# Kernel optimization log

Measured on AMD Instinct MI355X. Metric: run time of the kernel, lower is better.

Reference implementation:

```python
import jax, jax.numpy as jnp
import numpy as np

B, S, D, H = 2, 4096, 256, 4
DH = D // H  # head dim = 64


def setup_inputs() -> dict:
    key = jax.random.key(0)
    ks = jax.random.split(key, 7)
    scale = 1.0 / np.sqrt(D)
    return {
        "x": jax.random.normal(ks[0], (B, S, D), dtype=jnp.float32),
        "Wq": jax.random.normal(ks[1], (D, D), dtype=jnp.float32) * scale,
        "bq": jax.random.normal(ks[2], (D,), dtype=jnp.float32) * scale,
        "Wk": jax.random.normal(ks[3], (D, D), dtype=jnp.float32) * scale,
        "bk": jax.random.normal(ks[4], (D,), dtype=jnp.float32) * scale,
        "Wv": jax.random.normal(ks[5], (D, D), dtype=jnp.float32) * scale,
        "bv": jax.random.normal(ks[6], (D,), dtype=jnp.float32) * scale,
    }


def reference(x, Wq, bq, Wk, bk, Wv, bv):
    b, s, d = x.shape
    # torch Linear: y = x @ W.T + b ; W stored as [out, in]
    q = (jnp.einsum('bsd,ed->bse', x, Wq) + bq).reshape(b, s, H, DH)
    k = (jnp.einsum('bsd,ed->bse', x, Wk) + bk).reshape(b, s, H, DH)
    v = (jnp.einsum('bsd,ed->bse', x, Wv) + bv).reshape(b, s, H, DH)
    # scores: [b, s(query), t(key), h]
    scores = jnp.einsum('bshd,bthd->bsth', q, k) / jnp.sqrt(jnp.float32(DH))
    # softmax over key axis t (dim=-2 in torch layout bsth)
    weights = jax.nn.softmax(scores, axis=2)
    out = jnp.einsum('bsth,bthd->bshd', weights, v)
    return out.reshape(b, s, d)
```

## Files before the change

### kernel.cpp

```cpp
#include <hip/hip_runtime.h>

#define S_LEN 4096
#define D_MODEL 256
#define NH 4
#define DH 64
#define CSC 0.18033688011112042f
#define FRAG 520

typedef __attribute__((ext_vector_type(8))) short bf16x8;
typedef __attribute__((ext_vector_type(8))) unsigned short u16x8;
typedef __attribute__((ext_vector_type(4))) float f32x4;
typedef __attribute__((ext_vector_type(16))) float f32x16;
typedef __attribute__((ext_vector_type(2))) unsigned int u32x2;
typedef __attribute__((ext_vector_type(4))) unsigned int u32x4;

#define MFMA16(a, b, c) __builtin_amdgcn_mfma_f32_16x16x32_bf16((a), (b), (c), 0, 0, 0)
#define MFMA32(a, b, c) __builtin_amdgcn_mfma_f32_32x32x16_bf16((a), (b), (c), 0, 0, 0)

static __device__ __forceinline__ unsigned short f2bf(float f) {
  unsigned int u = __float_as_uint(f);
  u += 0x7fffu + ((u >> 16) & 1u);
  return (unsigned short)(u >> 16);
}

static __device__ __forceinline__ unsigned int cvtpk(float lo, float hi) {
  unsigned int r;
  asm("v_cvt_pk_bf16_f32 %0, %1, %2" : "=v"(r) : "v"(lo), "v"(hi));
  return r;
}

static __device__ __forceinline__ u16x8 cvt8(float4 a, float4 b) {
  u16x8 v;
  v[0] = f2bf(a.x); v[1] = f2bf(a.y); v[2] = f2bf(a.z); v[3] = f2bf(a.w);
  v[4] = f2bf(b.x); v[5] = f2bf(b.y); v[6] = f2bf(b.z); v[7] = f2bf(b.w);
  return v;
}

static __device__ __forceinline__ void pack_pb(const f32x16& s0, const f32x16& s1,
                                               bf16x8* pb) {
  unsigned int u0[8], u1[8];
#pragma unroll
  for (int gg = 0; gg < 4; ++gg) {
    u0[gg * 2 + 0] = cvtpk(s0[4 * gg + 0], s0[4 * gg + 1]);
    u0[gg * 2 + 1] = cvtpk(s0[4 * gg + 2], s0[4 * gg + 3]);
    u1[gg * 2 + 0] = cvtpk(s1[4 * gg + 0], s1[4 * gg + 1]);
    u1[gg * 2 + 1] = cvtpk(s1[4 * gg + 2], s1[4 * gg + 3]);
  }
#pragma unroll
  for (int S = 0; S < 2; ++S) {
    u32x2 w0 = __builtin_amdgcn_permlane32_swap(u0[4 * S + 0], u0[4 * S + 2], false, false);
    u32x2 w1 = __builtin_amdgcn_permlane32_swap(u0[4 * S + 1], u0[4 * S + 3], false, false);
    u32x4 t0; t0[0] = w0[0]; t0[1] = w1[0]; t0[2] = w0[1]; t0[3] = w1[1];
    pb[S] = __builtin_bit_cast(bf16x8, t0);
    u32x2 w2 = __builtin_amdgcn_permlane32_swap(u1[4 * S + 0], u1[4 * S + 2], false, false);
    u32x2 w3 = __builtin_amdgcn_permlane32_swap(u1[4 * S + 1], u1[4 * S + 3], false, false);
    u32x4 t1; t1[0] = w2[0]; t1[1] = w3[0]; t1[2] = w2[1]; t1[3] = w3[1];
    pb[2 + S] = __builtin_bit_cast(bf16x8, t1);
  }
}

__global__ __launch_bounds__(256) void prep(
    const float* __restrict__ Wq, const float* __restrict__ Wk,
    const float* __restrict__ Wv, unsigned short* __restrict__ Wb)
{
  const int gid = blockIdx.x * 256 + threadIdx.x;
  const int l   = gid & 63;
  const int f   = gid >> 6;
  const int kk  = f & 7;
  const int ctn = f >> 3;
  const int ct  = ctn & 3, nt = ctn >> 2;
  const int pj  = nt >> 2, h = nt & 3;
  const float* Wsel = (pj == 0) ? Wq : (pj == 1) ? Wk : Wv;
  const float* src =
      Wsel + (size_t)(h * 64 + ct * 16 + (l & 15)) * D_MODEL + kk * 32 + (l >> 4) * 8;
  float4 a = *(const float4*)src;
  float4 b = *(const float4*)(src + 4);
  *(u16x8*)(Wb + (size_t)gid * 8) = cvt8(a, b);
}

__global__ __launch_bounds__(256) void qkv_proj(
    const float* __restrict__ x, const unsigned short* __restrict__ Wb,
    const float* __restrict__ bq, const float* __restrict__ bk,
    const float* __restrict__ bv,
    unsigned short* __restrict__ Qh, unsigned short* __restrict__ Kh,
    unsigned short* __restrict__ Vt)
{
  __shared__ unsigned short xs[32][264];
  __shared__ float tbuf[32][68];

  const int tid  = threadIdx.x;
  const int lane = tid & 63;
  const int w    = tid >> 6;
  const int r16  = lane & 15;
  const int hi   = lane >> 4;
  const int m0   = (blockIdx.x >> 1) * 32;
  const int ntB  = (blockIdx.x & 1) * 6;

  {
    const int r  = tid >> 3;
    const int c0 = (tid & 7) * 32;
    const float* xp = x + (size_t)(m0 + r) * D_MODEL + c0;
#pragma unroll
    for (int i = 0; i < 32; i += 8) {
      float4 a = *(const float4*)(xp + i);
      float4 b = *(const float4*)(xp + i + 4);
      *(u16x8*)&xs[r][c0 + i] = cvt8(a, b);
    }
  }
  __syncthreads();

  const int bb = m0 >> 12;
  const int s_base = m0 & 4095;

  for (int t = 0; t < 6; ++t) {
    const int nt = ntB + t, pj = nt >> 2, h = nt & 3;
    f32x4 acc[2] = {};
    const size_t fb = (size_t)(nt * 4 + w) * 8;
#pragma unroll
    for (int kk = 0; kk < 8; ++kk) {
      bf16x8 bw = *(const bf16x8*)(Wb + (fb + kk) * 512 + lane * 8);
#pragma unroll
      for (int rt = 0; rt < 2; ++rt) {
        bf16x8 af = *(const bf16x8*)&xs[rt * 16 + r16][kk * 32 + hi * 8];
        acc[rt] = MFMA16(af, bw, acc[rt]);
      }
    }
    const float* bsel = (pj == 0) ? bq : (pj == 1) ? bk : bv;
    const float bias = bsel[h * 64 + w * 16 + r16];
    const float scl  = (pj == 0) ? CSC : 1.0f;

#pragma unroll
    for (int rt = 0; rt < 2; ++rt)
#pragma unroll
      for (int j = 0; j < 4; ++j)
        tbuf[rt * 16 + hi * 4 + j][w * 16 + r16] = (acc[rt][j] + bias) * scl;
    __syncthreads();

    if (pj < 2) {
      const int s_l = tid >> 3, c0 = (tid & 7) * 8;
      float4 a = *(const float4*)&tbuf[s_l][c0];
      float4 b = *(const float4*)&tbuf[s_l][c0 + 4];
      unsigned short* dst = ((pj == 0) ? Qh : Kh) +
          ((size_t)(bb * NH + h) * S_LEN + s_base + s_l) * DH + c0;
      *(u16x8*)dst = cvt8(a, b);
    } else {
      const int d_l = tid & 63, sblk = (tid >> 6) * 8;
      u16x8 vv;
#pragma unroll
      for (int e = 0; e < 8; ++e) vv[e] = f2bf(tbuf[sblk + e][d_l]);
      unsigned short* dst = Vt +
          ((size_t)(bb * NH + h) * DH + d_l) * S_LEN + s_base + sblk;
      *(u16x8*)dst = vv;
    }
    __syncthreads();
  }
}

__global__ __launch_bounds__(1024) void attn(
    const unsigned short* __restrict__ Qh,
    const unsigned short* __restrict__ Kh,
    const unsigned short* __restrict__ Vt,
    float* __restrict__ out)
{
  __shared__ unsigned short KV[2][2][4][8 * FRAG];

  const int tid = threadIdx.x;
  const int ln  = tid & 63;
  const int wv  = tid >> 6;
  const int g   = wv >> 2;
  const int wq  = wv & 3;
  const int r32 = ln & 31;
  const int h   = ln >> 5;

  const int bid = blockIdx.x;
  const int bh  = bid & 7;
  const int q0  = (bid >> 3) * 128;

  const unsigned short* Qb = Qh + (size_t)bh * S_LEN * DH;
  const unsigned short* Kb = Kh + (size_t)bh * S_LEN * DH;
  const unsigned short* Vb = Vt + (size_t)bh * DH * S_LEN;

  const int q = q0 + wq * 32 + r32;
  bf16x8 qf[4];
#pragma unroll
  for (int s = 0; s < 4; ++s)
    qf[s] = *(const bf16x8*)(Qb + (size_t)q * DH + s * 16 + h * 8);

  f32x16 o0 = {}, o1 = {};
  float l_run = 0.f;

  const int u  = tid & 255;
  const int gs = tid >> 8;
  const int sr = u >> 2;
  const int sc = (u & 3) * 16;
  const int f0   = (sc >> 4) * 2 + (sr >> 5);
  const int offA = f0 * FRAG + (sr & 31) * 8;
  const int offB = offA + 256;

  uint4 kA, kB, vA, vB;
#define LOAD_CHUNK(c)                                                          \
  { const unsigned short* kp = Kb + ((size_t)(c) * 64 + sr) * DH + sc;         \
    kA = *(const uint4*)kp;  kB = *(const uint4*)(kp + 8);                     \
    const unsigned short* vp = Vb + (size_t)sr * S_LEN + (c) * 64 + sc;        \
    vA = *(const uint4*)vp;  vB = *(const uint4*)(vp + 8); }
#define STAGE(par)                                                             \
  { unsigned short* kd = &KV[par][0][gs][0];                                   \
    *(uint4*)(kd + offA) = kA;  *(uint4*)(kd + offB) = kB;                     \
    unsigned short* vd = &KV[par][1][gs][0];                                   \
    *(uint4*)(vd + offA) = vA;  *(uint4*)(vd + offB) = vB; }

  LOAD_CHUNK(gs);
  STAGE(0);
  LOAD_CHUNK(4 + gs);

  for (int it = 0; it < 16; ++it) {
    __syncthreads();
    const unsigned short* Kc = &KV[it & 1][0][g][0];
    const unsigned short* Vc = &KV[it & 1][1][g][0];
    const int lb = ln * 8;

    f32x16 s0 = {}, s1 = {};
    __builtin_amdgcn_s_setprio(1);
#pragma unroll
    for (int s = 0; s < 4; ++s) {
      bf16x8 a0 = *(const bf16x8*)(Kc + lb + (2 * s + 0) * FRAG);
      bf16x8 a1 = *(const bf16x8*)(Kc + lb + (2 * s + 1) * FRAG);
      s0 = MFMA32(a0, qf[s], s0);
      s1 = MFMA32(a1, qf[s], s1);
    }
    __builtin_amdgcn_s_setprio(0);

    float pa = 0.f, pbs = 0.f, pc = 0.f, pd = 0.f;
#pragma unroll
    for (int i = 0; i < 16; i += 2) {
      s0[i]     = __builtin_amdgcn_exp2f(s0[i]);      pa  += s0[i];
      s0[i + 1] = __builtin_amdgcn_exp2f(s0[i + 1]);  pbs += s0[i + 1];
      s1[i]     = __builtin_amdgcn_exp2f(s1[i]);      pc  += s1[i];
      s1[i + 1] = __builtin_amdgcn_exp2f(s1[i + 1]);  pd  += s1[i + 1];
    }
    l_run += (pa + pbs) + (pc + pd);

    if (it < 15) {
      STAGE((it + 1) & 1);
      int c = 4 * (it + 2) + gs;  if (c > 63) c = 63;
      LOAD_CHUNK(c);
    }

    bf16x8 pb[4];
    pack_pb(s0, s1, pb);

    __builtin_amdgcn_s_setprio(1);
#pragma unroll
    for (int s = 0; s < 4; ++s) {
      bf16x8 b0 = *(const bf16x8*)(Vc + lb + (2 * s + 0) * FRAG);
      bf16x8 b1 = *(const bf16x8*)(Vc + lb + (2 * s + 1) * FRAG);
      o0 = MFMA32(b0, pb[s], o0);
      o1 = MFMA32(b1, pb[s], o1);
    }
    __builtin_amdgcn_s_setprio(0);
  }

  __syncthreads();
  float* cb = (float*)&KV[0][0][0][0];
  const int cbase = wq * 64 + ln;

  if (g >= 2) {
    const int base = ((g - 2) * 256 + cbase) * 33;
#pragma unroll
    for (int i = 0; i < 16; ++i) { cb[base + i] = o0[i]; cb[base + 16 + i] = o1[i]; }
    cb[base + 32] = l_run;
  }
  __syncthreads();
  if (g < 2) {
    const int base = (g * 256 + cbase) * 33;
#pragma unroll
    for (int i = 0; i < 16; ++i) { o0[i] += cb[base + i]; o1[i] += cb[base + 16 + i]; }
    l_run += cb[base + 32];
  }
  __syncthreads();
  if (g == 1) {
    const int base = cbase * 33;
#pragma unroll
    for (int i = 0; i < 16; ++i) { cb[base + i] = o0[i]; cb[base + 16 + i] = o1[i]; }
    cb[base + 32] = l_run;
  }
  __syncthreads();
  if (g == 0) {
    const int base = cbase * 33;
#pragma unroll
    for (int i = 0; i < 16; ++i) { o0[i] += cb[base + i]; o1[i] += cb[base + 16 + i]; }
    l_run += cb[base + 32];

    const float lt  = l_run + __shfl_xor(l_run, 32);
    const float inv = 1.f / lt;
    const int bb = bh >> 2, hd = bh & 3;
    float* op = out + ((size_t)(bb * S_LEN + q)) * D_MODEL + hd * DH;
#pragma unroll
    for (int gg = 0; gg < 4; ++gg) {
      float4 v0, v1;
      v0.x = o0[4 * gg + 0] * inv;  v0.y = o0[4 * gg + 1] * inv;
      v0.z = o0[4 * gg + 2] * inv;  v0.w = o0[4 * gg + 3] * inv;
      *(float4*)(op + 8 * gg + 4 * h) = v0;
      v1.x = o1[4 * gg + 0] * inv;  v1.y = o1[4 * gg + 1] * inv;
      v1.z = o1[4 * gg + 2] * inv;  v1.w = o1[4 * gg + 3] * inv;
      *(float4*)(op + 32 + 8 * gg + 4 * h) = v1;
    }
  }
}

extern "C" void kernel_launch(void* const* d_in, const int* in_sizes, int n_in,
                              void* d_out, int out_size, void* d_ws, size_t ws_size,
                              hipStream_t stream) {
  const float* x  = (const float*)d_in[0];
  const float* Wq = (const float*)d_in[1];
  const float* bq = (const float*)d_in[2];
  const float* Wk = (const float*)d_in[3];
  const float* bk = (const float*)d_in[4];
  const float* Wv = (const float*)d_in[5];
  const float* bv = (const float*)d_in[6];
  float* out = (float*)d_out;

  const size_t per = (size_t)2 * NH * S_LEN * DH;
  if (ws_size < 3 * per * sizeof(unsigned short)) return;
  unsigned short* Qh = (unsigned short*)d_ws;
  unsigned short* Kh = Qh + per;
  unsigned short* Vt = Kh + per;
  unsigned short* Wb = (unsigned short*)d_out;

  prep<<<96, 256, 0, stream>>>(Wq, Wk, Wv, Wb);
  qkv_proj<<<512, 256, 0, stream>>>(x, Wb, bq, bk, bv, Qh, Kh, Vt);
  attn<<<256, 1024, 0, stream>>>(Qh, Kh, Vt, out);
}
```

Before: 62.10 us.

## Split attention tile into halves to overlap exp/pack with MFMA; double qkv grid

The attention inner loop now computes the two 32-key score halves separately. It exponentiates and packs the first half and runs its PV MFMAs before doing the softmax of the second half, so transcendental work on one half can interleave with matrix ops on the other. The global-load staging is moved between the two halves. Separately, the QKV projection grid doubles to 1024 blocks, each handling 3 tiles instead of 6, which adds parallelism at the cost of reloading the x tile twice as often.

```diff
diff --git a/kernel.cpp b/kernel.cpp
--- a/kernel.cpp
+++ b/kernel.cpp
@@ -36,26 +36,19 @@
   return v;
 }
 
-static __device__ __forceinline__ void pack_pb(const f32x16& s0, const f32x16& s1,
-                                               bf16x8* pb) {
-  unsigned int u0[8], u1[8];
+static __device__ __forceinline__ void pack_half(const f32x16& s, bf16x8* pb) {
+  unsigned int u[8];
 #pragma unroll
   for (int gg = 0; gg < 4; ++gg) {
-    u0[gg * 2 + 0] = cvtpk(s0[4 * gg + 0], s0[4 * gg + 1]);
-    u0[gg * 2 + 1] = cvtpk(s0[4 * gg + 2], s0[4 * gg + 3]);
-    u1[gg * 2 + 0] = cvtpk(s1[4 * gg + 0], s1[4 * gg + 1]);
-    u1[gg * 2 + 1] = cvtpk(s1[4 * gg + 2], s1[4 * gg + 3]);
+    u[gg * 2 + 0] = cvtpk(s[4 * gg + 0], s[4 * gg + 1]);
+    u[gg * 2 + 1] = cvtpk(s[4 * gg + 2], s[4 * gg + 3]);
   }
 #pragma unroll
   for (int S = 0; S < 2; ++S) {
-    u32x2 w0 = __builtin_amdgcn_permlane32_swap(u0[4 * S + 0], u0[4 * S + 2], false, false);
-    u32x2 w1 = __builtin_amdgcn_permlane32_swap(u0[4 * S + 1], u0[4 * S + 3], false, false);
+    u32x2 w0 = __builtin_amdgcn_permlane32_swap(u[4 * S + 0], u[4 * S + 2], false, false);
+    u32x2 w1 = __builtin_amdgcn_permlane32_swap(u[4 * S + 1], u[4 * S + 3], false, false);
     u32x4 t0; t0[0] = w0[0]; t0[1] = w1[0]; t0[2] = w0[1]; t0[3] = w1[1];
     pb[S] = __builtin_bit_cast(bf16x8, t0);
-    u32x2 w2 = __builtin_amdgcn_permlane32_swap(u1[4 * S + 0], u1[4 * S + 2], false, false);
-    u32x2 w3 = __builtin_amdgcn_permlane32_swap(u1[4 * S + 1], u1[4 * S + 3], false, false);
-    u32x4 t1; t1[0] = w2[0]; t1[1] = w3[0]; t1[2] = w2[1]; t1[3] = w3[1];
-    pb[2 + S] = __builtin_bit_cast(bf16x8, t1);
   }
 }
 
@@ -93,8 +86,8 @@
   const int w    = tid >> 6;
   const int r16  = lane & 15;
   const int hi   = lane >> 4;
-  const int m0   = (blockIdx.x >> 1) * 32;
-  const int ntB  = (blockIdx.x & 1) * 6;
+  const int m0   = (blockIdx.x >> 2) * 32;
+  const int ntB  = (blockIdx.x & 3) * 3;
 
   {
     const int r  = tid >> 3;
@@ -112,7 +105,7 @@
   const int bb = m0 >> 12;
   const int s_base = m0 & 4095;
 
-  for (int t = 0; t < 6; ++t) {
+  for (int t = 0; t < 3; ++t) {
     const int nt = ntB + t, pj = nt >> 2, h = nt & 3;
     f32x4 acc[2] = {};
     const size_t fb = (size_t)(nt * 4 + w) * 8;
@@ -219,26 +212,45 @@
     const unsigned short* Vc = &KV[it & 1][1][g][0];
     const int lb = ln * 8;
 
-    f32x16 s0 = {}, s1 = {};
+    f32x16 s0 = {};
     __builtin_amdgcn_s_setprio(1);
 #pragma unroll
     for (int s = 0; s < 4; ++s) {
       bf16x8 a0 = *(const bf16x8*)(Kc + lb + (2 * s + 0) * FRAG);
+      s0 = MFMA32(a0, qf[s], s0);
+    }
+    __builtin_amdgcn_s_setprio(0);
+
+    f32x16 s1 = {};
+    __builtin_amdgcn_s_setprio(1);
+#pragma unroll
+    for (int s = 0; s < 4; ++s) {
       bf16x8 a1 = *(const bf16x8*)(Kc + lb + (2 * s + 1) * FRAG);
-      s0 = MFMA32(a0, qf[s], s0);
       s1 = MFMA32(a1, qf[s], s1);
     }
     __builtin_amdgcn_s_setprio(0);
 
-    float pa = 0.f, pbs = 0.f, pc = 0.f, pd = 0.f;
-#pragma unroll
-    for (int i = 0; i < 16; i += 2) {
-      s0[i]     = __builtin_amdgcn_exp2f(s0[i]);      pa  += s0[i];
-      s0[i + 1] = __builtin_amdgcn_exp2f(s0[i + 1]);  pbs += s0[i + 1];
-      s1[i]     = __builtin_amdgcn_exp2f(s1[i]);      pc  += s1[i];
-      s1[i + 1] = __builtin_amdgcn_exp2f(s1[i + 1]);  pd  += s1[i + 1];
-    }
-    l_run += (pa + pbs) + (pc + pd);
+    {
+      float pa = 0.f, pbs = 0.f;
+#pragma unroll
+      for (int i = 0; i < 16; i += 2) {
+        s0[i]     = __builtin_amdgcn_exp2f(s0[i]);      pa  += s0[i];
+        s0[i + 1] = __builtin_amdgcn_exp2f(s0[i + 1]);  pbs += s0[i + 1];
+      }
+      l_run += pa + pbs;
+    }
+    bf16x8 p01[2];
+    pack_half(s0, p01);
+
+    __builtin_amdgcn_s_setprio(1);
+#pragma unroll
+    for (int s = 0; s < 2; ++s) {
+      bf16x8 b0 = *(const bf16x8*)(Vc + lb + (2 * s + 0) * FRAG);
+      bf16x8 b1 = *(const bf16x8*)(Vc + lb + (2 * s + 1) * FRAG);
+      o0 = MFMA32(b0, p01[s], o0);
+      o1 = MFMA32(b1, p01[s], o1);
+    }
+    __builtin_amdgcn_s_setprio(0);
 
     if (it < 15) {
       STAGE((it + 1) & 1);
@@ -246,16 +258,25 @@
       LOAD_CHUNK(c);
     }
 
-    bf16x8 pb[4];
-    pack_pb(s0, s1, pb);
+    {
+      float pa = 0.f, pbs = 0.f;
+#pragma unroll
+      for (int i = 0; i < 16; i += 2) {
+        s1[i]     = __builtin_amdgcn_exp2f(s1[i]);      pa  += s1[i];
+        s1[i + 1] = __builtin_amdgcn_exp2f(s1[i + 1]);  pbs += s1[i + 1];
+      }
+      l_run += pa + pbs;
+    }
+    bf16x8 p23[2];
+    pack_half(s1, p23);
 
     __builtin_amdgcn_s_setprio(1);
 #pragma unroll
-    for (int s = 0; s < 4; ++s) {
-      bf16x8 b0 = *(const bf16x8*)(Vc + lb + (2 * s + 0) * FRAG);
-      bf16x8 b1 = *(const bf16x8*)(Vc + lb + (2 * s + 1) * FRAG);
-      o0 = MFMA32(b0, pb[s], o0);
-      o1 = MFMA32(b1, pb[s], o1);
+    for (int s = 0; s < 2; ++s) {
+      bf16x8 b0 = *(const bf16x8*)(Vc + lb + (4 + 2 * s) * FRAG);
+      bf16x8 b1 = *(const bf16x8*)(Vc + lb + (5 + 2 * s) * FRAG);
+      o0 = MFMA32(b0, p23[s], o0);
+      o1 = MFMA32(b1, p23[s], o1);
     }
     __builtin_amdgcn_s_setprio(0);
   }
@@ -328,6 +349,6 @@
   unsigned short* Wb = (unsigned short*)d_out;
 
   prep<<<96, 256, 0, stream>>>(Wq, Wk, Wv, Wb);
-  qkv_proj<<<512, 256, 0, stream>>>(x, Wb, bq, bk, bv, Qh, Kh, Vt);
+  qkv_proj<<<1024, 256, 0, stream>>>(x, Wb, bq, bk, bv, Qh, Kh, Vt);
   attn<<<256, 1024, 0, stream>>>(Qh, Kh, Vt, out);
 }
```

Measured after the change: 62.86 us. About the same (+1.2%).
